# Kernel optimization log

Hardware: AMD Instinct MI355X
Metric: run time of the kernel (lower is better)

## Reference

```python
import jax, jax.numpy as jnp
import numpy as np

H = 1024  # hidden_size == embedding_size


def setup_inputs() -> dict:
    key = jax.random.key(0)
    ks = jax.random.split(key, 14)
    B, T, L, V = 2, 1, 8192, 50000
    emb_table = jax.random.normal(ks[0], (V, H), jnp.float32)
    emb_table = emb_table.at[0].set(0.0)  # row 0 zeroed as in the torch module
    return {
        "input_ids": jax.random.randint(ks[1], (B, T), 0, V),
        "last_context": jax.random.normal(ks[2], (B, T, H), jnp.float32),
        "last_hidden": jax.random.normal(ks[3], (1, B, H), jnp.float32),
        "encoder_outputs": jax.random.normal(ks[4], (B, L, H), jnp.float32),
        "emb_table": emb_table,
        "w_ih": jax.random.normal(ks[5], (3 * H, 2 * H), jnp.float32) * 0.02,
        "w_hh": jax.random.normal(ks[6], (3 * H, H), jnp.float32) * 0.02,
        "b_ih": jax.random.normal(ks[7], (3 * H,), jnp.float32) * 0.02,
        "b_hh": jax.random.normal(ks[8], (3 * H,), jnp.float32) * 0.02,
        "attn_w": jax.random.normal(ks[9], (H, 2 * H), jnp.float32) * 0.02,
        "attn_b": jax.random.normal(ks[10], (H,), jnp.float32) * 0.02,
        "v": jax.random.normal(ks[11], (H,), jnp.float32),
        "out_w": jax.random.normal(ks[12], (50000, 2 * H), jnp.float32) * 0.02,
        "out_b": jax.random.normal(ks[13], (50000,), jnp.float32) * 0.02,
    }


def _forward(input_ids, last_context, last_hidden, encoder_outputs, emb_table,
             w_ih, w_hh, b_ih, b_hh, attn_w, attn_b, v, out_w, out_b):
    # Embedding lookup (dropout p=0 -> identity)
    embedded = emb_table[input_ids]                      # [B,1,H]
    rnn_in = jnp.concatenate([embedded, last_context], -1)  # [B,1,2H]

    # Single-step, single-layer GRU (torch gate order: r, z, n)
    x = rnn_in[:, 0]                                     # [B,2H]
    h = last_hidden[0]                                   # [B,H]
    gx = x @ w_ih.T + b_ih                               # [B,3H]
    gh = h @ w_hh.T + b_hh                               # [B,3H]
    r = jax.nn.sigmoid(gx[:, :H] + gh[:, :H])
    z = jax.nn.sigmoid(gx[:, H:2 * H] + gh[:, H:2 * H])
    n = jnp.tanh(gx[:, 2 * H:] + r * gh[:, 2 * H:])
    h_new = (1.0 - z) * n + z * h                        # [B,H]
    rnn_output = h_new[:, None, :]                       # [B,1,H]
    hidden = h_new[None]                                 # [1,B,H]

    # Bahdanau 'concat' attention, vectorized over the seq_len loop:
    # energy[b,i] = v . (attn_w @ concat(h_new[b], enc[b,i]) + attn_b)
    w_h, w_e = attn_w[:, :H], attn_w[:, H:]
    e_h = h_new @ w_h.T + attn_b                         # [B,H]
    e_e = jnp.einsum('blh,kh->blk', encoder_outputs, w_e)  # [B,L,H]
    energies = jnp.einsum('blk,k->bl', e_e + e_h[:, None, :], v)  # [B,L]
    attn_weights = jax.nn.softmax(energies, axis=1)      # [B,L]
    context = jnp.einsum('bl,blh->bh', attn_weights, encoder_outputs)[:, None, :]  # [B,1,H]

    # Output projection over concat(rnn_output, context)
    cat = jnp.concatenate([rnn_output, context], -1)     # [B,1,2H]
    output = cat @ out_w.T + out_b                       # [B,1,V]
    return output, context, hidden, embedded, rnn_output


def reference(input_ids, last_context, last_hidden, encoder_outputs, emb_table,
              w_ih, w_hh, b_ih, b_hh, attn_w, attn_b, v, out_w, out_b):
    return _forward(input_ids, last_context, last_hidden, encoder_outputs, emb_table,
                    w_ih, w_hh, b_ih, b_hh, attn_w, attn_b, v, out_w, out_b)
```

## Files before the change

kernel.cpp:

```cpp
#include <hip/hip_runtime.h>

#define H 1024
#define B2 2
#define LEN 8192
#define V 50000

__device__ __forceinline__ float dot4(float4 a, float4 b) {
    return a.x * b.x + a.y * b.y + a.z * b.z + a.w * b.w;
}

__global__ void k_upart(const float* __restrict__ attn_w,
                        const float* __restrict__ v,
                        float* __restrict__ upart) {
    int h  = blockIdx.x * 256 + threadIdx.x;
    int kc = blockIdx.y;
    float acc = 0.f;
#pragma unroll 8
    for (int i = 0; i < 64; ++i) {
        int k = kc * 64 + i;
        acc += v[k] * attn_w[(long)k * (2 * H) + H + h];
    }
    upart[kc * H + h] = acc;
}

__global__ void k_ured_emb(const float* __restrict__ upart,
                           float* __restrict__ u,
                           const int* __restrict__ ids,
                           const float* __restrict__ emb,
                           float* __restrict__ out_emb) {
    int h = blockIdx.x * 256 + threadIdx.x;
    float acc = 0.f;
#pragma unroll
    for (int kc = 0; kc < 16; ++kc) acc += upart[kc * H + h];
    u[h] = acc;
    out_emb[h]     = emb[(long)ids[0] * H + h];
    out_emb[H + h] = emb[(long)ids[1] * H + h];
}

__global__ void k_gru(const int* __restrict__ ids,
                      const float* __restrict__ emb,
                      const float* __restrict__ lctx,
                      const float* __restrict__ lhid,
                      const float* __restrict__ w_ih,
                      const float* __restrict__ w_hh,
                      const float* __restrict__ b_ih,
                      const float* __restrict__ b_hh,
                      float* __restrict__ o_hidden,
                      float* __restrict__ o_rnn) {
    int hh = blockIdx.x;
    int t  = threadIdx.x;
    int kb = t * 8;

    float4 x0a, x0b, x1a, x1b;
    if (kb < H) {
        const float* p0 = emb + (long)ids[0] * H + kb;
        const float* p1 = emb + (long)ids[1] * H + kb;
        x0a = *(const float4*)p0;       x0b = *(const float4*)(p0 + 4);
        x1a = *(const float4*)p1;       x1b = *(const float4*)(p1 + 4);
    } else {
        const float* p0 = lctx + (kb - H);
        const float* p1 = lctx + H + (kb - H);
        x0a = *(const float4*)p0;       x0b = *(const float4*)(p0 + 4);
        x1a = *(const float4*)p1;       x1b = *(const float4*)(p1 + 4);
    }
    int kb2 = t * 4;
    float4 h0 = *(const float4*)(lhid + kb2);
    float4 h1 = *(const float4*)(lhid + H + kb2);

    __shared__ float lds[3][4][4];
    for (int g = 0; g < 3; ++g) {
        const float* wi = w_ih + ((long)g * H + hh) * (2 * H) + kb;
        const float* wh = w_hh + ((long)g * H + hh) * H + kb2;
        float4 wa = *(const float4*)wi;
        float4 wb = *(const float4*)(wi + 4);
        float4 wc = *(const float4*)wh;
        float a0 = dot4(wa, x0a) + dot4(wb, x0b);
        float a1 = dot4(wa, x1a) + dot4(wb, x1b);
        float c0 = dot4(wc, h0);
        float c1 = dot4(wc, h1);
        for (int off = 32; off; off >>= 1) {
            a0 += __shfl_down(a0, off, 64);
            a1 += __shfl_down(a1, off, 64);
            c0 += __shfl_down(c0, off, 64);
            c1 += __shfl_down(c1, off, 64);
        }
        if ((t & 63) == 0) {
            int w = t >> 6;
            lds[g][w][0] = a0; lds[g][w][1] = a1;
            lds[g][w][2] = c0; lds[g][w][3] = c1;
        }
    }
    __syncthreads();
    if (t == 0) {
        float gx[3][2], gh[3][2];
        for (int g = 0; g < 3; ++g) {
            float s0 = 0, s1 = 0, s2 = 0, s3 = 0;
            for (int w = 0; w < 4; ++w) {
                s0 += lds[g][w][0]; s1 += lds[g][w][1];
                s2 += lds[g][w][2]; s3 += lds[g][w][3];
            }
            float bi = b_ih[g * H + hh], bh = b_hh[g * H + hh];
            gx[g][0] = s0 + bi; gx[g][1] = s1 + bi;
            gh[g][0] = s2 + bh; gh[g][1] = s3 + bh;
        }
        for (int b = 0; b < B2; ++b) {
            float r  = 1.f / (1.f + expf(-(gx[0][b] + gh[0][b])));
            float z  = 1.f / (1.f + expf(-(gx[1][b] + gh[1][b])));
            float n  = tanhf(gx[2][b] + r * gh[2][b]);
            float hp = lhid[b * H + hh];
            float hn = (1.f - z) * n + z * hp;
            o_hidden[b * H + hh] = hn;
            o_rnn[b * H + hh]    = hn;
        }
    }
}

__global__ void k_energy(const float* __restrict__ enc,
                         const float* __restrict__ u,
                         float* __restrict__ en) {
    int row  = (blockIdx.x << 2) + (threadIdx.x >> 6);
    int lane = threadIdx.x & 63;
    const float* e = enc + (long)row * H;
    float acc = 0.f;
#pragma unroll
    for (int c = 0; c < 4; ++c) {
        int k = c * 256 + lane * 4;
        float4 ev = *(const float4*)(e + k);
        float4 uv = *(const float4*)(u + k);
        acc += dot4(ev, uv);
    }
    for (int off = 32; off; off >>= 1) acc += __shfl_down(acc, off, 64);
    if (lane == 0) en[row] = acc;
}

__global__ void k_softmax(float* __restrict__ en) {
    int b = blockIdx.x;
    float* e = en + b * LEN;
    int t = threadIdx.x;
    __shared__ float lds[16];
    float vals[8];
    float m = -3.4e38f;
#pragma unroll
    for (int i = 0; i < 8; ++i) { vals[i] = e[i * 1024 + t]; m = fmaxf(m, vals[i]); }
    for (int off = 32; off; off >>= 1) m = fmaxf(m, __shfl_xor(m, off, 64));
    if ((t & 63) == 0) lds[t >> 6] = m;
    __syncthreads();
    m = lds[0];
#pragma unroll
    for (int w = 1; w < 16; ++w) m = fmaxf(m, lds[w]);
    __syncthreads();
    float s = 0.f;
#pragma unroll
    for (int i = 0; i < 8; ++i) { vals[i] = expf(vals[i] - m); s += vals[i]; }
    for (int off = 32; off; off >>= 1) s += __shfl_xor(s, off, 64);
    if ((t & 63) == 0) lds[t >> 6] = s;
    __syncthreads();
    float tot = 0.f;
#pragma unroll
    for (int w = 0; w < 16; ++w) tot += lds[w];
    float inv = 1.f / tot;
#pragma unroll
    for (int i = 0; i < 8; ++i) e[i * 1024 + t] = vals[i] * inv;
}

__global__ void k_ctx_part(const float* __restrict__ enc,
                           const float* __restrict__ p,
                           float* __restrict__ part) {
    int b  = blockIdx.x >> 7;
    int lc = blockIdx.x & 127;
    int t  = threadIdx.x;
    const float* e  = enc + ((long)b * LEN + lc * 64) * H + t * 4;
    const float* pw = p + b * LEN + lc * 64;
    float4 acc = {0.f, 0.f, 0.f, 0.f};
#pragma unroll 4
    for (int i = 0; i < 64; ++i) {
        float w = pw[i];
        float4 ev = *(const float4*)(e + (long)i * H);
        acc.x += w * ev.x; acc.y += w * ev.y; acc.z += w * ev.z; acc.w += w * ev.w;
    }
    *(float4*)(part + (long)blockIdx.x * H + t * 4) = acc;
}

__global__ void k_ctx_red(const float* __restrict__ part,
                          float* __restrict__ out_ctx) {
    int idx = blockIdx.x * 256 + threadIdx.x;
    int b = idx >> 10, h = idx & 1023;
    float acc = 0.f;
#pragma unroll 8
    for (int lc = 0; lc < 128; ++lc) acc += part[((b << 7) + lc) * H + h];
    out_ctx[idx] = acc;
}

__global__ void k_out(const float* __restrict__ ow,
                      const float* __restrict__ ob,
                      const float* __restrict__ hnew,
                      const float* __restrict__ ctx,
                      float* __restrict__ out) {
    int t  = threadIdx.x;
    int kb = t * 8;
    float c0[8], c1[8];
#pragma unroll
    for (int i = 0; i < 8; ++i) {
        int k = kb + i;
        c0[i] = (k < H) ? hnew[k]     : ctx[k - H];
        c1[i] = (k < H) ? hnew[H + k] : ctx[k];
    }
    __shared__ float lds[4][2];
    long obase = (long)blockIdx.x * 8;
    for (int r = 0; r < 8; ++r) {
        long o = obase + r;
        const float4* w4 = (const float4*)(ow + o * (2 * H) + kb);
        float4 wa = w4[0], wb = w4[1];
        float a0 = wa.x * c0[0] + wa.y * c0[1] + wa.z * c0[2] + wa.w * c0[3]
                 + wb.x * c0[4] + wb.y * c0[5] + wb.z * c0[6] + wb.w * c0[7];
        float a1 = wa.x * c1[0] + wa.y * c1[1] + wa.z * c1[2] + wa.w * c1[3]
                 + wb.x * c1[4] + wb.y * c1[5] + wb.z * c1[6] + wb.w * c1[7];
        for (int off = 32; off; off >>= 1) {
            a0 += __shfl_down(a0, off, 64);
            a1 += __shfl_down(a1, off, 64);
        }
        int wave = t >> 6, lane = t & 63;
        if (lane == 0) { lds[wave][0] = a0; lds[wave][1] = a1; }
        __syncthreads();
        if (t == 0) {
            float s0 = lds[0][0] + lds[1][0] + lds[2][0] + lds[3][0];
            float s1 = lds[0][1] + lds[1][1] + lds[2][1] + lds[3][1];
            float bb = ob[o];
            out[o]     = s0 + bb;
            out[V + o] = s1 + bb;
        }
        __syncthreads();
    }
}

extern "C" void kernel_launch(void* const* d_in, const int* in_sizes, int n_in,
                              void* d_out, int out_size, void* d_ws, size_t ws_size,
                              hipStream_t stream) {
    const int*   ids    = (const int*)  d_in[0];
    const float* lctx   = (const float*)d_in[1];
    const float* lhid   = (const float*)d_in[2];
    const float* enc    = (const float*)d_in[3];
    const float* emb    = (const float*)d_in[4];
    const float* w_ih   = (const float*)d_in[5];
    const float* w_hh   = (const float*)d_in[6];
    const float* b_ih   = (const float*)d_in[7];
    const float* b_hh   = (const float*)d_in[8];
    const float* attn_w = (const float*)d_in[9];
    const float* v      = (const float*)d_in[11];
    const float* out_w  = (const float*)d_in[12];
    const float* out_b  = (const float*)d_in[13];

    float* out_f       = (float*)d_out;
    float* o_output    = out_f;
    float* o_context   = out_f + 100000;
    float* o_hidden    = out_f + 102048;
    float* o_embedded  = out_f + 104096;
    float* o_rnn       = out_f + 106144;

    float* ws    = (float*)d_ws;
    float* U     = ws;
    float* UPART = ws + 1024;
    float* EN    = ws + 17408;
    float* PART  = ws + 33792;

    k_upart   <<<dim3(4, 16), 256, 0, stream>>>(attn_w, v, UPART);
    k_ured_emb<<<4,            256, 0, stream>>>(UPART, U, ids, emb, o_embedded);
    k_gru     <<<1024,         256, 0, stream>>>(ids, emb, lctx, lhid, w_ih, w_hh,
                                                 b_ih, b_hh, o_hidden, o_rnn);
    k_energy  <<<4096,         256, 0, stream>>>(enc, U, EN);
    k_softmax <<<2,           1024, 0, stream>>>(EN);
    k_ctx_part<<<256,          256, 0, stream>>>(enc, EN, PART);
    k_ctx_red <<<8,            256, 0, stream>>>(PART, o_context);
    k_out     <<<6250,         256, 0, stream>>>(out_w, out_b, o_hidden, o_context,
                                                 o_output);
}
```

Before: 133.8 us.

## Fuse launches, merge GRU with energy, fold softmax into context, restructure output GEMV

Merges the u-partial and embedding-copy kernels, and runs the GRU and attention-energy work in one grid. The softmax is folded into each context block, so every block recomputes the row max and sum over all 8192 energies. The output projection now gives each wave a whole row with no block-level syncs, using twice as many blocks. This cuts the number of launches and the barrier overhead in the output GEMV, at the cost of redundant softmax reductions in all 256 context blocks.

```diff
diff --git a/kernel.cpp b/kernel.cpp
--- a/kernel.cpp
+++ b/kernel.cpp
@@ -9,46 +9,74 @@
     return a.x * b.x + a.y * b.y + a.z * b.z + a.w * b.w;
 }
 
-__global__ void k_upart(const float* __restrict__ attn_w,
-                        const float* __restrict__ v,
-                        float* __restrict__ upart) {
-    int h  = blockIdx.x * 256 + threadIdx.x;
-    int kc = blockIdx.y;
-    float acc = 0.f;
+__global__ void k_upart_emb(const float* __restrict__ attn_w,
+                            const float* __restrict__ v,
+                            float* __restrict__ upart,
+                            const int* __restrict__ ids,
+                            const float* __restrict__ emb,
+                            float* __restrict__ out_emb) {
+    int bid = blockIdx.x;
+    int t   = threadIdx.x;
+    if (bid < 64) {
+        int h  = (bid & 3) * 256 + t;
+        int kc = bid >> 2;
+        float acc = 0.f;
 #pragma unroll 8
-    for (int i = 0; i < 64; ++i) {
-        int k = kc * 64 + i;
-        acc += v[k] * attn_w[(long)k * (2 * H) + H + h];
-    }
-    upart[kc * H + h] = acc;
-}
-
-__global__ void k_ured_emb(const float* __restrict__ upart,
-                           float* __restrict__ u,
-                           const int* __restrict__ ids,
-                           const float* __restrict__ emb,
-                           float* __restrict__ out_emb) {
+        for (int i = 0; i < 64; ++i) {
+            int k = kc * 64 + i;
+            acc += v[k] * attn_w[(long)k * (2 * H) + H + h];
+        }
+        upart[kc * H + h] = acc;
+    } else {
+        int idx = (bid - 64) * 256 + t;
+        int b = idx >> 10, h = idx & 1023;
+        out_emb[idx] = emb[(long)ids[b] * H + h];
+    }
+}
+
+__global__ void k_ured(const float* __restrict__ upart,
+                       float* __restrict__ u) {
     int h = blockIdx.x * 256 + threadIdx.x;
     float acc = 0.f;
 #pragma unroll
     for (int kc = 0; kc < 16; ++kc) acc += upart[kc * H + h];
     u[h] = acc;
-    out_emb[h]     = emb[(long)ids[0] * H + h];
-    out_emb[H + h] = emb[(long)ids[1] * H + h];
-}
-
-__global__ void k_gru(const int* __restrict__ ids,
-                      const float* __restrict__ emb,
-                      const float* __restrict__ lctx,
-                      const float* __restrict__ lhid,
-                      const float* __restrict__ w_ih,
-                      const float* __restrict__ w_hh,
-                      const float* __restrict__ b_ih,
-                      const float* __restrict__ b_hh,
-                      float* __restrict__ o_hidden,
-                      float* __restrict__ o_rnn) {
+}
+
+__global__ void k_gru_energy(const int* __restrict__ ids,
+                             const float* __restrict__ emb,
+                             const float* __restrict__ lctx,
+                             const float* __restrict__ lhid,
+                             const float* __restrict__ w_ih,
+                             const float* __restrict__ w_hh,
+                             const float* __restrict__ b_ih,
+                             const float* __restrict__ b_hh,
+                             const float* __restrict__ enc,
+                             const float* __restrict__ u,
+                             float* __restrict__ o_hidden,
+                             float* __restrict__ o_rnn,
+                             float* __restrict__ en) {
+    __shared__ float lds[3][4][4];
+    int t = threadIdx.x;
+
+    if (blockIdx.x >= 1024) {
+        int row  = ((blockIdx.x - 1024) << 2) + (t >> 6);
+        int lane = t & 63;
+        const float* e = enc + (long)row * H;
+        float acc = 0.f;
+#pragma unroll
+        for (int c = 0; c < 4; ++c) {
+            int k = c * 256 + lane * 4;
+            float4 ev = *(const float4*)(e + k);
+            float4 uv = *(const float4*)(u + k);
+            acc += dot4(ev, uv);
+        }
+        for (int off = 32; off; off >>= 1) acc += __shfl_down(acc, off, 64);
+        if (lane == 0) en[row] = acc;
+        return;
+    }
+
     int hh = blockIdx.x;
-    int t  = threadIdx.x;
     int kb = t * 8;
 
     float4 x0a, x0b, x1a, x1b;
@@ -67,7 +95,6 @@
     float4 h0 = *(const float4*)(lhid + kb2);
     float4 h1 = *(const float4*)(lhid + H + kb2);
 
-    __shared__ float lds[3][4][4];
     for (int g = 0; g < 3; ++g) {
         const float* wi = w_ih + ((long)g * H + hh) * (2 * H) + kb;
         const float* wh = w_hh + ((long)g * H + hh) * H + kb2;
@@ -115,66 +142,40 @@
     }
 }
 
-__global__ void k_energy(const float* __restrict__ enc,
-                         const float* __restrict__ u,
-                         float* __restrict__ en) {
-    int row  = (blockIdx.x << 2) + (threadIdx.x >> 6);
-    int lane = threadIdx.x & 63;
-    const float* e = enc + (long)row * H;
-    float acc = 0.f;
-#pragma unroll
-    for (int c = 0; c < 4; ++c) {
-        int k = c * 256 + lane * 4;
-        float4 ev = *(const float4*)(e + k);
-        float4 uv = *(const float4*)(u + k);
-        acc += dot4(ev, uv);
-    }
-    for (int off = 32; off; off >>= 1) acc += __shfl_down(acc, off, 64);
-    if (lane == 0) en[row] = acc;
-}
-
-__global__ void k_softmax(float* __restrict__ en) {
-    int b = blockIdx.x;
-    float* e = en + b * LEN;
-    int t = threadIdx.x;
-    __shared__ float lds[16];
-    float vals[8];
-    float m = -3.4e38f;
-#pragma unroll
-    for (int i = 0; i < 8; ++i) { vals[i] = e[i * 1024 + t]; m = fmaxf(m, vals[i]); }
-    for (int off = 32; off; off >>= 1) m = fmaxf(m, __shfl_xor(m, off, 64));
-    if ((t & 63) == 0) lds[t >> 6] = m;
-    __syncthreads();
-    m = lds[0];
-#pragma unroll
-    for (int w = 1; w < 16; ++w) m = fmaxf(m, lds[w]);
-    __syncthreads();
-    float s = 0.f;
-#pragma unroll
-    for (int i = 0; i < 8; ++i) { vals[i] = expf(vals[i] - m); s += vals[i]; }
-    for (int off = 32; off; off >>= 1) s += __shfl_xor(s, off, 64);
-    if ((t & 63) == 0) lds[t >> 6] = s;
-    __syncthreads();
-    float tot = 0.f;
-#pragma unroll
-    for (int w = 0; w < 16; ++w) tot += lds[w];
-    float inv = 1.f / tot;
-#pragma unroll
-    for (int i = 0; i < 8; ++i) e[i * 1024 + t] = vals[i] * inv;
-}
-
-__global__ void k_ctx_part(const float* __restrict__ enc,
-                           const float* __restrict__ p,
-                           float* __restrict__ part) {
+__global__ void k_ctx(const float* __restrict__ enc,
+                      const float* __restrict__ en,
+                      float* __restrict__ part) {
     int b  = blockIdx.x >> 7;
     int lc = blockIdx.x & 127;
     int t  = threadIdx.x;
-    const float* e  = enc + ((long)b * LEN + lc * 64) * H + t * 4;
-    const float* pw = p + b * LEN + lc * 64;
+    const float* e_row = en + b * LEN;
+
+    __shared__ float red[4];
+    __shared__ float wlds[64];
+
+    float m = -3.4e38f;
+    for (int i = t; i < LEN; i += 256) m = fmaxf(m, e_row[i]);
+    for (int off = 32; off; off >>= 1) m = fmaxf(m, __shfl_xor(m, off, 64));
+    if ((t & 63) == 0) red[t >> 6] = m;
+    __syncthreads();
+    m = fmaxf(fmaxf(red[0], red[1]), fmaxf(red[2], red[3]));
+
+    float s = 0.f;
+    for (int i = t; i < LEN; i += 256) s += expf(e_row[i] - m);
+    for (int off = 32; off; off >>= 1) s += __shfl_xor(s, off, 64);
+    __syncthreads();
+    if ((t & 63) == 0) red[t >> 6] = s;
+    __syncthreads();
+    float inv = 1.f / (red[0] + red[1] + red[2] + red[3]);
+
+    if (t < 64) wlds[t] = expf(e_row[lc * 64 + t] - m) * inv;
+    __syncthreads();
+
+    const float* e = enc + ((long)b * LEN + lc * 64) * H + t * 4;
     float4 acc = {0.f, 0.f, 0.f, 0.f};
 #pragma unroll 4
     for (int i = 0; i < 64; ++i) {
-        float w = pw[i];
+        float w = wlds[i];
         float4 ev = *(const float4*)(e + (long)i * H);
         acc.x += w * ev.x; acc.y += w * ev.y; acc.z += w * ev.z; acc.w += w * ev.w;
     }
@@ -196,40 +197,41 @@
                       const float* __restrict__ hnew,
                       const float* __restrict__ ctx,
                       float* __restrict__ out) {
-    int t  = threadIdx.x;
-    int kb = t * 8;
-    float c0[8], c1[8];
-#pragma unroll
-    for (int i = 0; i < 8; ++i) {
-        int k = kb + i;
-        c0[i] = (k < H) ? hnew[k]     : ctx[k - H];
-        c1[i] = (k < H) ? hnew[H + k] : ctx[k];
-    }
-    __shared__ float lds[4][2];
-    long obase = (long)blockIdx.x * 8;
-    for (int r = 0; r < 8; ++r) {
-        long o = obase + r;
-        const float4* w4 = (const float4*)(ow + o * (2 * H) + kb);
-        float4 wa = w4[0], wb = w4[1];
-        float a0 = wa.x * c0[0] + wa.y * c0[1] + wa.z * c0[2] + wa.w * c0[3]
-                 + wb.x * c0[4] + wb.y * c0[5] + wb.z * c0[6] + wb.w * c0[7];
-        float a1 = wa.x * c1[0] + wa.y * c1[1] + wa.z * c1[2] + wa.w * c1[3]
-                 + wb.x * c1[4] + wb.y * c1[5] + wb.z * c1[6] + wb.w * c1[7];
-        for (int off = 32; off; off >>= 1) {
-            a0 += __shfl_down(a0, off, 64);
-            a1 += __shfl_down(a1, off, 64);
-        }
-        int wave = t >> 6, lane = t & 63;
-        if (lane == 0) { lds[wave][0] = a0; lds[wave][1] = a1; }
-        __syncthreads();
-        if (t == 0) {
-            float s0 = lds[0][0] + lds[1][0] + lds[2][0] + lds[3][0];
-            float s1 = lds[0][1] + lds[1][1] + lds[2][1] + lds[3][1];
-            float bb = ob[o];
-            out[o]     = s0 + bb;
-            out[V + o] = s1 + bb;
-        }
-        __syncthreads();
+    int t    = threadIdx.x;
+    int lane = t & 63;
+    int wv   = t >> 6;
+    long row = (long)blockIdx.x * 4 + wv;
+
+    float4 c0[8], c1[8];
+#pragma unroll
+    for (int j = 0; j < 4; ++j) {
+        int k = (lane + 64 * j) * 4;
+        c0[j] = *(const float4*)(hnew + k);
+        c1[j] = *(const float4*)(hnew + H + k);
+    }
+#pragma unroll
+    for (int j = 4; j < 8; ++j) {
+        int k = (lane + 64 * j) * 4 - H;
+        c0[j] = *(const float4*)(ctx + k);
+        c1[j] = *(const float4*)(ctx + H + k);
+    }
+
+    const float4* w4 = (const float4*)(ow + row * (2 * H));
+    float a0 = 0.f, a1 = 0.f;
+#pragma unroll
+    for (int j = 0; j < 8; ++j) {
+        float4 w = w4[lane + 64 * j];
+        a0 += dot4(w, c0[j]);
+        a1 += dot4(w, c1[j]);
+    }
+    for (int off = 32; off; off >>= 1) {
+        a0 += __shfl_down(a0, off, 64);
+        a1 += __shfl_down(a1, off, 64);
+    }
+    if (lane == 0) {
+        float bb = ob[row];
+        out[row]     = a0 + bb;
+        out[V + row] = a1 + bb;
     }
 }
 
@@ -263,14 +265,13 @@
     float* EN    = ws + 17408;
     float* PART  = ws + 33792;
 
-    k_upart   <<<dim3(4, 16), 256, 0, stream>>>(attn_w, v, UPART);
-    k_ured_emb<<<4,            256, 0, stream>>>(UPART, U, ids, emb, o_embedded);
-    k_gru     <<<1024,         256, 0, stream>>>(ids, emb, lctx, lhid, w_ih, w_hh,
-                                                 b_ih, b_hh, o_hidden, o_rnn);
-    k_energy  <<<4096,         256, 0, stream>>>(enc, U, EN);
-    k_softmax <<<2,           1024, 0, stream>>>(EN);
-    k_ctx_part<<<256,          256, 0, stream>>>(enc, EN, PART);
-    k_ctx_red <<<8,            256, 0, stream>>>(PART, o_context);
-    k_out     <<<6250,         256, 0, stream>>>(out_w, out_b, o_hidden, o_context,
-                                                 o_output);
-}
+    k_upart_emb <<<72,    256, 0, stream>>>(attn_w, v, UPART, ids, emb, o_embedded);
+    k_ured      <<<4,     256, 0, stream>>>(UPART, U);
+    k_gru_energy<<<5120,  256, 0, stream>>>(ids, emb, lctx, lhid, w_ih, w_hh,
+                                            b_ih, b_hh, enc, U,
+                                            o_hidden, o_rnn, EN);
+    k_ctx       <<<256,   256, 0, stream>>>(enc, EN, PART);
+    k_ctx_red   <<<8,     256, 0, stream>>>(PART, o_context);
+    k_out       <<<12500, 256, 0, stream>>>(out_w, out_b, o_hidden, o_context,
+                                            o_output);
+}
```

After: 131.6 us. Within noise of the previous version (-1.6%).
